# Kernel optimization log

Hardware: AMD Instinct MI355X
Metric: run time of the kernel (lower is better)

Reference implementation:

```python
import jax, jax.numpy as jnp
import numpy as np

N = 1048576  # total points
B = 64       # number of clouds in batch
D = 64       # feature dim


def _make_lengths():
    rng = np.random.RandomState(0)
    w = rng.rand(B) + 0.5
    lengths = np.floor(w / w.sum() * N).astype(np.int64)
    lengths[-1] += N - lengths.sum()  # make lengths sum exactly to N
    return lengths


def setup_inputs() -> dict:
    key = jax.random.key(0)
    x = jax.random.normal(key, (N, D), dtype=jnp.float32)
    lengths_np = _make_lengths()
    segment_ids = jnp.asarray(np.repeat(np.arange(B, dtype=np.int64), lengths_np))
    lengths = jnp.asarray(lengths_np)
    return {"x": x, "segment_ids": segment_ids, "lengths": lengths}


def reference(x, segment_ids, lengths):
    # fused segmented mean: one pass over x instead of B separate mean kernels
    sums = jax.ops.segment_sum(x, segment_ids, num_segments=B)  # [B, D]
    return sums / lengths.astype(x.dtype)[:, None]
```

## Files before the change

kernel.cpp:

```cpp
#include <hip/hip_runtime.h>


#define D 64
#define ROWS_PER_BLOCK 512
#define NTHREADS 256

typedef float f32x4 __attribute__((ext_vector_type(4)));

__global__ __launch_bounds__(NTHREADS) void seg_sum_kernel(
    const float* __restrict__ x,
    const int*   __restrict__ seg,
    const int*   __restrict__ len,
    float*       __restrict__ out,
    int n_rows, int B)
{
    __shared__ float lacc[2][D];

    const int tid = threadIdx.x;
    const int r0  = blockIdx.x * ROWS_PER_BLOCK;
    if (r0 >= n_rows) return;
    int r1 = r0 + ROWS_PER_BLOCK;
    if (r1 > n_rows) r1 = n_rows;

    const int col     = (tid & 15) * 4;
    const int rowlane = tid >> 4;
    const int lane    = tid & 63;

    const bool full = (r1 - r0) == ROWS_PER_BLOCK;

    int mylen = 0;
    if (B <= 64 && lane < B) mylen = len[lane];

    const float* p = x + (size_t)(r0 + rowlane) * D + col;
    f32x4 w0{}, w1{}, w2{}, w3{}, w4{}, w5{}, w6{}, w7{};
    if (full) {
        w0 = *(const f32x4*)(p + (size_t)0 * 16 * D);
        w1 = *(const f32x4*)(p + (size_t)1 * 16 * D);
        w2 = *(const f32x4*)(p + (size_t)2 * 16 * D);
        w3 = *(const f32x4*)(p + (size_t)3 * 16 * D);
        w4 = *(const f32x4*)(p + (size_t)4 * 16 * D);
        w5 = *(const f32x4*)(p + (size_t)5 * 16 * D);
        w6 = *(const f32x4*)(p + (size_t)6 * 16 * D);
        w7 = *(const f32x4*)(p + (size_t)7 * 16 * D);
    }

    int s0, nb, boundary = r1;
    if (B <= 64) {
        int incl = mylen;
        #pragma unroll
        for (int d = 1; d < 64; d <<= 1) {
            const int t = __shfl_up(incl, d, 64);
            if (lane >= d) incl += t;
        }
        const int o_beg = incl - mylen;
        s0 = __popcll(__ballot(o_beg <= r0)) - 1;
        const unsigned long long mb = __ballot(o_beg > r0 && o_beg < r1);
        nb = __popcll(mb);
        if (nb) boundary = __shfl(o_beg, (int)(__ffsll((long long)mb) - 1), 64);
    } else {
        s0 = seg[r0];
        nb = (seg[r1 - 1] != s0) ? 2 : 0;
    }

    if (nb <= 1) {
        f32x4 a0 = {0.f, 0.f, 0.f, 0.f};
        f32x4 a1 = {0.f, 0.f, 0.f, 0.f};

        if (full && nb == 0) {
            f32x4 t0 = w0, t1 = w1, t2 = w2, t3 = w3;
            t0 += w4; t1 += w5; t2 += w6; t3 += w7;
            #pragma unroll
            for (int it = 1; it < 4; ++it) {
                const float* q = p + (size_t)it * 128 * D;
                const f32x4 v0 = *(const f32x4*)(q + (size_t)0 * 16 * D);
                const f32x4 v1 = *(const f32x4*)(q + (size_t)1 * 16 * D);
                const f32x4 v2 = *(const f32x4*)(q + (size_t)2 * 16 * D);
                const f32x4 v3 = *(const f32x4*)(q + (size_t)3 * 16 * D);
                const f32x4 v4 = *(const f32x4*)(q + (size_t)4 * 16 * D);
                const f32x4 v5 = *(const f32x4*)(q + (size_t)5 * 16 * D);
                const f32x4 v6 = *(const f32x4*)(q + (size_t)6 * 16 * D);
                const f32x4 v7 = *(const f32x4*)(q + (size_t)7 * 16 * D);
                t0 += v0; t1 += v1; t2 += v2; t3 += v3;
                t0 += v4; t1 += v5; t2 += v6; t3 += v7;
            }
            a0 = (t0 + t1) + (t2 + t3);
        } else if (full) {
            const int rbase = r0 + rowlane;
            if (rbase +   0 < boundary) a0 += w0; else a1 += w0;
            if (rbase +  16 < boundary) a0 += w1; else a1 += w1;
            if (rbase +  32 < boundary) a0 += w2; else a1 += w2;
            if (rbase +  48 < boundary) a0 += w3; else a1 += w3;
            if (rbase +  64 < boundary) a0 += w4; else a1 += w4;
            if (rbase +  80 < boundary) a0 += w5; else a1 += w5;
            if (rbase +  96 < boundary) a0 += w6; else a1 += w6;
            if (rbase + 112 < boundary) a0 += w7; else a1 += w7;
            #pragma unroll 8
            for (int r = rbase + 128; r < r1; r += 16) {
                const f32x4 v = *(const f32x4*)(x + (size_t)r * D + col);
                if (r < boundary) { a0 += v; } else { a1 += v; }
            }
        } else {
            for (int r = r0 + rowlane; r < r1; r += 16) {
                const f32x4 v = *(const f32x4*)(x + (size_t)r * D + col);
                if (r < boundary) { a0 += v; } else { a1 += v; }
            }
        }

        for (int i = tid; i < 2 * D; i += NTHREADS) ((float*)lacc)[i] = 0.0f;
        __syncthreads();
        atomicAdd(&lacc[0][col + 0], a0.x);
        atomicAdd(&lacc[0][col + 1], a0.y);
        atomicAdd(&lacc[0][col + 2], a0.z);
        atomicAdd(&lacc[0][col + 3], a0.w);
        if (nb) {
            atomicAdd(&lacc[1][col + 0], a1.x);
            atomicAdd(&lacc[1][col + 1], a1.y);
            atomicAdd(&lacc[1][col + 2], a1.z);
            atomicAdd(&lacc[1][col + 3], a1.w);
        }
        __syncthreads();
        if (tid < D) {
            atomicAdd(&out[(size_t)s0 * D + tid], lacc[0][tid]);
            if (nb)
                atomicAdd(&out[(size_t)(s0 + 1) * D + tid], lacc[1][tid]);
        }
    } else {
        f32x4 a = {0.f, 0.f, 0.f, 0.f};
        int cur = -1;
        for (int r = r0 + rowlane; r < r1; r += 16) {
            const int s = seg[r];
            const f32x4 v = *(const f32x4*)(x + (size_t)r * D + col);
            if (s != cur) {
                if (cur >= 0) {
                    atomicAdd(&out[(size_t)cur * D + col + 0], a.x);
                    atomicAdd(&out[(size_t)cur * D + col + 1], a.y);
                    atomicAdd(&out[(size_t)cur * D + col + 2], a.z);
                    atomicAdd(&out[(size_t)cur * D + col + 3], a.w);
                }
                a = {0.f, 0.f, 0.f, 0.f};
                cur = s;
            }
            a += v;
        }
        if (cur >= 0) {
            atomicAdd(&out[(size_t)cur * D + col + 0], a.x);
            atomicAdd(&out[(size_t)cur * D + col + 1], a.y);
            atomicAdd(&out[(size_t)cur * D + col + 2], a.z);
            atomicAdd(&out[(size_t)cur * D + col + 3], a.w);
        }
    }
}

__global__ __launch_bounds__(NTHREADS) void seg_div_kernel(
    const int* __restrict__ len,
    float*     __restrict__ out,
    int total)
{
    const int i = blockIdx.x * blockDim.x + threadIdx.x;
    if (i < total) {
        out[i] = out[i] / (float)len[i >> 6];
    }
}

extern "C" void kernel_launch(void* const* d_in, const int* in_sizes, int n_in,
                              void* d_out, int out_size, void* d_ws, size_t ws_size,
                              hipStream_t stream) {
    const float* x   = (const float*)d_in[0];
    const int*   seg = (const int*)d_in[1];
    const int*   len = (const int*)d_in[2];
    float*       out = (float*)d_out;

    const int n_rows = in_sizes[1];
    const int B      = in_sizes[2];
    const int total  = B * D;

    hipMemsetAsync(out, 0, (size_t)total * sizeof(float), stream);

    const int grid = (n_rows + ROWS_PER_BLOCK - 1) / ROWS_PER_BLOCK;
    seg_sum_kernel<<<grid, NTHREADS, 0, stream>>>(x, seg, len, out, n_rows, B);

    const int grid2 = (total + NTHREADS - 1) / NTHREADS;
    seg_div_kernel<<<grid2, NTHREADS, 0, stream>>>(len, out, total);
}
```

Before: 363.1 us.

## Double rows per block and replace LDS atomics with shuffle-based wave reduction

Each block now processes 1024 rows instead of 512, which halves the number of blocks and the global atomics issued to the output. The block reduction uses __shfl_xor within each wave, then per-wave shared arrays summed by a single thread per column, instead of shared-memory atomics. The two-segment flush now spreads over 128 threads. For B>64 the code no longer reads seg to find s0; it forces the general path (nb=2), which changes behaviour for large B.

Result: no change. 357.9 us (-1.4%).

```diff
diff --git a/kernel.cpp b/kernel.cpp
--- a/kernel.cpp
+++ b/kernel.cpp
@@ -2,7 +2,7 @@
 
 
 #define D 64
-#define ROWS_PER_BLOCK 512
+#define ROWS_PER_BLOCK 1024
 #define NTHREADS 256
 
 typedef float f32x4 __attribute__((ext_vector_type(4)));
@@ -14,7 +14,8 @@
     float*       __restrict__ out,
     int n_rows, int B)
 {
-    __shared__ float lacc[2][D];
+    __shared__ float l0[4][D];
+    __shared__ float l1[4][D];
 
     const int tid = threadIdx.x;
     const int r0  = blockIdx.x * ROWS_PER_BLOCK;
@@ -25,6 +26,7 @@
     const int col     = (tid & 15) * 4;
     const int rowlane = tid >> 4;
     const int lane    = tid & 63;
+    const int wid     = tid >> 6;
 
     const bool full = (r1 - r0) == ROWS_PER_BLOCK;
 
@@ -44,7 +46,7 @@
         w7 = *(const f32x4*)(p + (size_t)7 * 16 * D);
     }
 
-    int s0, nb, boundary = r1;
+    int s0 = 0, nb = 2, boundary = r1;
     if (B <= 64) {
         int incl = mylen;
         #pragma unroll
@@ -57,9 +59,6 @@
         const unsigned long long mb = __ballot(o_beg > r0 && o_beg < r1);
         nb = __popcll(mb);
         if (nb) boundary = __shfl(o_beg, (int)(__ffsll((long long)mb) - 1), 64);
-    } else {
-        s0 = seg[r0];
-        nb = (seg[r1 - 1] != s0) ? 2 : 0;
     }
 
     if (nb <= 1) {
@@ -70,7 +69,7 @@
             f32x4 t0 = w0, t1 = w1, t2 = w2, t3 = w3;
             t0 += w4; t1 += w5; t2 += w6; t3 += w7;
             #pragma unroll
-            for (int it = 1; it < 4; ++it) {
+            for (int it = 1; it < 8; ++it) {
                 const float* q = p + (size_t)it * 128 * D;
                 const f32x4 v0 = *(const f32x4*)(q + (size_t)0 * 16 * D);
                 const f32x4 v1 = *(const f32x4*)(q + (size_t)1 * 16 * D);
@@ -106,23 +105,34 @@
             }
         }
 
-        for (int i = tid; i < 2 * D; i += NTHREADS) ((float*)lacc)[i] = 0.0f;
-        __syncthreads();
-        atomicAdd(&lacc[0][col + 0], a0.x);
-        atomicAdd(&lacc[0][col + 1], a0.y);
-        atomicAdd(&lacc[0][col + 2], a0.z);
-        atomicAdd(&lacc[0][col + 3], a0.w);
+        #pragma unroll
+        for (int j = 0; j < 4; ++j) {
+            a0[j] += __shfl_xor(a0[j], 16, 64);
+            a0[j] += __shfl_xor(a0[j], 32, 64);
+        }
         if (nb) {
-            atomicAdd(&lacc[1][col + 0], a1.x);
-            atomicAdd(&lacc[1][col + 1], a1.y);
-            atomicAdd(&lacc[1][col + 2], a1.z);
-            atomicAdd(&lacc[1][col + 3], a1.w);
+            #pragma unroll
+            for (int j = 0; j < 4; ++j) {
+                a1[j] += __shfl_xor(a1[j], 16, 64);
+                a1[j] += __shfl_xor(a1[j], 32, 64);
+            }
+        }
+        if (lane < 16) {
+            #pragma unroll
+            for (int j = 0; j < 4; ++j) l0[wid][lane * 4 + j] = a0[j];
+            if (nb) {
+                #pragma unroll
+                for (int j = 0; j < 4; ++j) l1[wid][lane * 4 + j] = a1[j];
+            }
         }
         __syncthreads();
         if (tid < D) {
-            atomicAdd(&out[(size_t)s0 * D + tid], lacc[0][tid]);
-            if (nb)
-                atomicAdd(&out[(size_t)(s0 + 1) * D + tid], lacc[1][tid]);
+            const float s = (l0[0][tid] + l0[1][tid]) + (l0[2][tid] + l0[3][tid]);
+            atomicAdd(&out[(size_t)s0 * D + tid], s);
+        } else if (nb && tid < 2 * D) {
+            const int c = tid - D;
+            const float s = (l1[0][c] + l1[1][c]) + (l1[2][c] + l1[3][c]);
+            atomicAdd(&out[(size_t)(s0 + 1) * D + c], s);
         }
     } else {
         f32x4 a = {0.f, 0.f, 0.f, 0.f};
```
